# Performance work log

Measured on AMD Instinct MI355X. Metric: run time of the kernel, lower is better.

## Reference

```python
import jax, jax.numpy as jnp
import numpy as np

G = 4          # moe_groups
EPG = 4        # experts per group = e_num // moe_groups
E = 16         # e_num
KG = 2         # moe_max_groups
K = 2          # moe_max_k
GTP = 0.9      # moe_group_top_p
TP = 0.9       # moe_top_p
SCALE = 1.0 / float(np.sqrt(G))  # group_scale


def setup_inputs() -> dict:
    key = jax.random.key(0)
    ks = jax.random.split(key, 6)
    B, T, D, H = 2, 1024, 512, 2048  # H = 4*emb_dim per SwiGLU_FFN(emb_dim, 4*emb_dim)
    x = jax.random.normal(ks[0], (B, T, D), jnp.float32)
    Wr = jax.random.normal(ks[1], (D, G), jnp.float32) * 0.02      # group_router weight
    br = jnp.zeros((G,), jnp.float32)                               # group_router bias
    Wgate = jax.random.normal(ks[2], (G, D, EPG), jnp.float32) * 0.02  # per-group gates
    bgate = jnp.zeros((G, EPG), jnp.float32)
    W1 = jax.random.normal(ks[3], (E, D, H), jnp.float32) * 0.02   # SwiGLU gate proj
    W3 = jax.random.normal(ks[4], (E, D, H), jnp.float32) * 0.02   # SwiGLU up proj
    W2 = jax.random.normal(ks[5], (E, H, D), jnp.float32) * 0.02   # SwiGLU down proj
    return {"x": x, "Wr": Wr, "br": br, "Wgate": Wgate, "bgate": bgate,
            "W1": W1, "W3": W3, "W2": W2}


def _routing_weights(xf, Wr, br, Wgate, bgate):
    # Returns combined per-(token, expert) weight (N, E): group_renorm * expert_renorm * SCALE.
    N = xf.shape[0]
    # ---- group-level top-p routing ----
    gp = jax.nn.softmax(xf @ Wr + br, axis=-1)                      # (N, G)
    order = jnp.argsort(-gp, axis=-1)
    sp_k = jnp.take_along_axis(gp, order, axis=-1)[:, :KG]          # top-KG probs, descending
    idx_k = order[:, :KG]
    act = jnp.cumsum(sp_k, axis=-1) <= GTP
    act = act.at[:, 0].set(True)                                    # always keep best group
    mp = sp_k * act
    rn = mp / (jnp.sum(mp, axis=-1, keepdims=True) + 1e-9)
    w_group = jnp.zeros((N, G), xf.dtype).at[jnp.arange(N)[:, None], idx_k].set(rn)
    # ---- expert-level top-p routing within each group ----
    ep = jax.nn.softmax(jnp.einsum('nd,gde->nge', xf, Wgate) + bgate, axis=-1)  # (N, G, EPG)
    eorder = jnp.argsort(-ep, axis=-1)
    esp = jnp.take_along_axis(ep, eorder, axis=-1)[:, :, :K]
    eidx = eorder[:, :, :K]
    eact = jnp.cumsum(esp, axis=-1) <= TP
    eact = eact.at[:, :, 0].set(True)                               # always keep best expert
    emp = esp * eact
    ern = emp / (jnp.sum(emp, axis=-1, keepdims=True) + 1e-9)
    w_exp = jnp.zeros((N, G, EPG), xf.dtype).at[
        jnp.arange(N)[:, None, None], jnp.arange(G)[None, :, None], eidx].set(ern)
    return (w_group[:, :, None] * w_exp * SCALE).reshape(N, E)      # (N, E)


def reference(x, Wr, br, Wgate, bgate, W1, W3, W2):
    B, T, D = x.shape
    xf = x.reshape(-1, D)                                           # (N, D)
    tw = _routing_weights(xf, Wr, br, Wgate, bgate)                 # (N, E)
    out = jnp.zeros_like(xf)
    for e in range(E):  # fixed structural loop over experts
        h = jax.nn.silu(xf @ W1[e]) * (xf @ W3[e])                  # SwiGLU hidden (N, H)
        out = out + tw[:, e:e + 1] * (h @ W2[e])
    return out.reshape(B, T, D)
```

## Files before the change

kernel.cpp:

```cpp
#include <hip/hip_runtime.h>
#include <math.h>

typedef unsigned short u16;
typedef unsigned int   u32;
typedef short s16x8 __attribute__((ext_vector_type(8)));
typedef float f32x4 __attribute__((ext_vector_type(4)));

#define N_TOK 2048
#define DIM   512
#define HID   2048
#define NE    16
#define NG    4
#define EPG   4
#define MAXT  2048

#define BM 64
#define BN 128
#define BK 64

#define WS_CNT    0
#define WS_OFF    128
#define WS_TOKIDX 256
#define WS_TW     (WS_TOKIDX + NE*MAXT*4)
#define WS_XB     (WS_TW + N_TOK*NE*4)
#define WS_HBUF   (WS_XB + (size_t)N_TOK*DIM*2)
#define WS_W1T    (WS_HBUF + (size_t)8192*HID*2)
#define WS_W3T    (WS_W1T + (size_t)NE*HID*DIM*2)
#define WS_W2T    (WS_W3T + (size_t)NE*HID*DIM*2)

__device__ __forceinline__ int* ws_i32(void* ws, size_t off) { return (int*)((char*)ws + off); }

__device__ __forceinline__ u16 f2b(float f) {
    union { float f; u32 i; } v; v.f = f;
    u32 b = v.i;
    u32 r = b + 0x7FFFu + ((b >> 16) & 1u);
    return (u16)(r >> 16);
}

__device__ __forceinline__ void gl_lds16(const u16* g, u16* l) {
    __builtin_amdgcn_global_load_lds((const __attribute__((address_space(1))) void*)g,
                                     (__attribute__((address_space(3))) void*)l, 16, 0, 0);
}

__global__ __launch_bounds__(256) void routing_kernel(
    const float* __restrict__ x, const float* __restrict__ Wr, const float* __restrict__ br,
    const float* __restrict__ Wgate, const float* __restrict__ bgate, void* ws)
{
    int tid = threadIdx.x;
    int t = blockIdx.x * 4 + (tid >> 6);
    int lane = tid & 63;

    float xl[8];
    {
        const float4* xr = (const float4*)(x + (size_t)t*DIM + lane*8);
        float4 a = xr[0], b = xr[1];
        xl[0]=a.x; xl[1]=a.y; xl[2]=a.z; xl[3]=a.w;
        xl[4]=b.x; xl[5]=b.y; xl[6]=b.z; xl[7]=b.w;
    }

    {
        union { u16 h[8]; uint4 q; } pk;
        #pragma unroll
        for (int i = 0; i < 8; i++) pk.h[i] = f2b(xl[i]);
        u16* xb = (u16*)((char*)ws + WS_XB);
        *(uint4*)(xb + (size_t)t*DIM + lane*8) = pk.q;
    }

    float gl[NG] = {0.f,0.f,0.f,0.f};
    float el[NE];
    #pragma unroll
    for (int e = 0; e < NE; e++) el[e] = 0.f;

    {
        const float4* Wr4 = (const float4*)Wr;
        #pragma unroll
        for (int c = 0; c < 8; c++) {
            float4 w = Wr4[lane*8 + c];
            gl[0] += xl[c]*w.x; gl[1] += xl[c]*w.y;
            gl[2] += xl[c]*w.z; gl[3] += xl[c]*w.w;
        }
    }
    {
        const float4* Wg4 = (const float4*)Wgate;
        #pragma unroll
        for (int g = 0; g < NG; g++) {
            #pragma unroll
            for (int c = 0; c < 8; c++) {
                float4 w = Wg4[(size_t)g*DIM + lane*8 + c];
                el[g*4+0] += xl[c]*w.x; el[g*4+1] += xl[c]*w.y;
                el[g*4+2] += xl[c]*w.z; el[g*4+3] += xl[c]*w.w;
            }
        }
    }

    #pragma unroll
    for (int g = 0; g < NG; g++)
        #pragma unroll
        for (int s = 32; s; s >>= 1) gl[g] += __shfl_xor(gl[g], s);
    #pragma unroll
    for (int e = 0; e < NE; e++)
        #pragma unroll
        for (int s = 32; s; s >>= 1) el[e] += __shfl_xor(el[e], s);

    if (lane != 0) return;

    float gp[NG];
    float mx = -1e30f;
    #pragma unroll
    for (int g = 0; g < NG; g++) { gl[g] += br[g]; mx = fmaxf(mx, gl[g]); }
    float sum = 0.f;
    #pragma unroll
    for (int g = 0; g < NG; g++) { gp[g] = expf(gl[g] - mx); sum += gp[g]; }
    #pragma unroll
    for (int g = 0; g < NG; g++) gp[g] /= sum;

    int i0 = 0;
    #pragma unroll
    for (int g = 1; g < NG; g++) if (gp[g] > gp[i0]) i0 = g;
    int i1 = -1;
    #pragma unroll
    for (int g = 0; g < NG; g++) { if (g == i0) continue; if (i1 < 0 || gp[g] > gp[i1]) i1 = g; }

    bool act1 = (gp[i0] + gp[i1]) <= 0.9f;
    float mp0 = gp[i0], mp1 = act1 ? gp[i1] : 0.f;
    float inv = 1.f / (mp0 + mp1 + 1e-9f);
    float wg[NG] = {0.f,0.f,0.f,0.f};
    wg[i0] = mp0 * inv;
    wg[i1] = mp1 * inv;

    float tw[NE];
    #pragma unroll
    for (int g = 0; g < NG; g++) {
        float ep[EPG];
        float emx = -1e30f;
        #pragma unroll
        for (int j = 0; j < EPG; j++) {
            float v = el[g*4 + j] + bgate[g*4 + j];
            ep[j] = v; emx = fmaxf(emx, v);
        }
        float es = 0.f;
        #pragma unroll
        for (int j = 0; j < EPG; j++) { ep[j] = expf(ep[j] - emx); es += ep[j]; }
        #pragma unroll
        for (int j = 0; j < EPG; j++) ep[j] /= es;

        int j0 = 0;
        #pragma unroll
        for (int j = 1; j < EPG; j++) if (ep[j] > ep[j0]) j0 = j;
        int j1 = -1;
        #pragma unroll
        for (int j = 0; j < EPG; j++) { if (j == j0) continue; if (j1 < 0 || ep[j] > ep[j1]) j1 = j; }

        bool ea1 = (ep[j0] + ep[j1]) <= 0.9f;
        float e0 = ep[j0], e1 = ea1 ? ep[j1] : 0.f;
        float einv = 1.f / (e0 + e1 + 1e-9f);
        float we[EPG] = {0.f,0.f,0.f,0.f};
        we[j0] = e0 * einv;
        we[j1] = e1 * einv;
        #pragma unroll
        for (int j = 0; j < EPG; j++) tw[g*4 + j] = wg[g] * we[j] * 0.5f;
    }

    float* twT = (float*)((char*)ws + WS_TW);
    #pragma unroll
    for (int e = 0; e < NE; e++) twT[(size_t)e*N_TOK + t] = tw[e];
}

__global__ __launch_bounds__(1024) void expert_scan_kernel(void* ws)
{
    int tid = threadIdx.x;
    int e = tid >> 6, lane = tid & 63;
    const float* twT = (const float*)((char*)ws + WS_TW) + (size_t)e*N_TOK;
    int* tok = ws_i32(ws, WS_TOKIDX) + e*MAXT;
    __shared__ int scnt[NE];

    float v[32];
    #pragma unroll
    for (int r = 0; r < 32; r++) v[r] = twT[r*64 + lane];

    unsigned long long lanemask = (1ull << lane) - 1ull;
    int base = 0;
    #pragma unroll
    for (int r = 0; r < 32; r++) {
        bool a = v[r] > 0.f;
        unsigned long long m = __ballot(a);
        if (a) tok[base + __popcll(m & lanemask)] = r*64 + lane;
        base += __popcll(m);
    }
    if (lane == 0) scnt[e] = base;
    __syncthreads();
    if (tid == 0) {
        int* cnt = ws_i32(ws, WS_CNT);
        int* off = ws_i32(ws, WS_OFF);
        int s = 0;
        for (int i = 0; i < NE; i++) { cnt[i] = scnt[i]; off[i] = s; s += scnt[i]; }
        off[NE] = s;
    }
}

__global__ __launch_bounds__(256) void transpose_all_kernel(
    const float* __restrict__ W1, const float* __restrict__ W3,
    const float* __restrict__ W2, void* ws)
{
    int z = blockIdx.z;
    int mat = z >> 4, e = z & 15;
    const float* src; u16* dst; int K, N, k0, n0;
    if (mat == 0)      { src = W1; dst = (u16*)((char*)ws + WS_W1T); K = DIM; N = HID; n0 = blockIdx.x*64; k0 = blockIdx.y*64; }
    else if (mat == 1) { src = W3; dst = (u16*)((char*)ws + WS_W3T); K = DIM; N = HID; n0 = blockIdx.x*64; k0 = blockIdx.y*64; }
    else               { src = W2; dst = (u16*)((char*)ws + WS_W2T); K = HID; N = DIM; k0 = blockIdx.x*64; n0 = blockIdx.y*64; }

    const float* s = src + (size_t)e*K*N;
    u16* d = dst + (size_t)e*N*K;

    __shared__ u16 T[64*64];
    int tid = threadIdx.x;
    int j = tid & 15, i = tid >> 4;

    {
        const float* base = s + (size_t)(k0 + 4*i)*N + n0 + 4*j;
        float4 v0 = *(const float4*)(base);
        float4 v1 = *(const float4*)(base + N);
        float4 v2 = *(const float4*)(base + 2*N);
        float4 v3 = *(const float4*)(base + 3*N);
        int swz = (j & 7) << 1;
        int pc = 4 * (i ^ swz);
        union { u16 h[4]; uint2 q; } p;
        p.h[0]=f2b(v0.x); p.h[1]=f2b(v1.x); p.h[2]=f2b(v2.x); p.h[3]=f2b(v3.x);
        *(uint2*)(&T[(4*j+0)*64 + pc]) = p.q;
        p.h[0]=f2b(v0.y); p.h[1]=f2b(v1.y); p.h[2]=f2b(v2.y); p.h[3]=f2b(v3.y);
        *(uint2*)(&T[(4*j+1)*64 + pc]) = p.q;
        p.h[0]=f2b(v0.z); p.h[1]=f2b(v1.z); p.h[2]=f2b(v2.z); p.h[3]=f2b(v3.z);
        *(uint2*)(&T[(4*j+2)*64 + pc]) = p.q;
        p.h[0]=f2b(v0.w); p.h[1]=f2b(v1.w); p.h[2]=f2b(v2.w); p.h[3]=f2b(v3.w);
        *(uint2*)(&T[(4*j+3)*64 + pc]) = p.q;
    }
    __syncthreads();
    #pragma unroll
    for (int it = 0; it < 2; it++) {
        int idx = tid + it*256;
        int nr = idx >> 3, sg = idx & 7;
        int p = (2*sg) ^ (((nr >> 2) & 7) << 1);
        *(s16x8*)(d + (size_t)(n0+nr)*K + k0 + sg*8) = *(const s16x8*)(&T[nr*64 + 4*p]);
    }
}

__global__ __launch_bounds__(256) void gemm1_fast(void* ws)
{
    int e  = blockIdx.z;
    const int* cnt = ws_i32(ws, WS_CNT);
    int ce = cnt[e];
    int m0 = blockIdx.y * BM;
    if (m0 >= ce) return;
    int n0 = blockIdx.x * BN;

    const int* off = ws_i32(ws, WS_OFF);
    const int* tok = ws_i32(ws, WS_TOKIDX) + e*MAXT;
    const u16* xb  = (const u16*)((char*)ws + WS_XB);
    const u16* W1T = (const u16*)((char*)ws + WS_W1T) + (size_t)e*HID*DIM;
    const u16* W3T = (const u16*)((char*)ws + WS_W3T) + (size_t)e*HID*DIM;
    u16* hbuf = (u16*)((char*)ws + WS_HBUF);
    int obase = off[e] + m0;

    __shared__ u16 As[BM*BK];
    __shared__ u16 Bs0[BN*BK];
    __shared__ u16 Bs1[BN*BK];
    __shared__ int rowtok[BM];

    int tid = threadIdx.x;
    if (tid < BM) {
        int m = m0 + tid;
        rowtok[tid] = tok[m < ce ? m : (ce - 1)];
    }
    __syncthreads();

    int wave = tid >> 6, lane = tid & 63;
    int quad = lane >> 4, l16 = lane & 15;
    int swz  = l16 & 7;
    int r8 = lane >> 3, sg = lane & 7;
    int swk = ((sg ^ r8) << 3);

    const u16* arow0 = xb + (size_t)rowtok[wave*16 + r8]*DIM + swk;
    const u16* arow1 = xb + (size_t)rowtok[wave*16 + 8 + r8]*DIM + swk;
    const u16* b1row[4]; const u16* b3row[4];
    #pragma unroll
    for (int i = 0; i < 4; i++) {
        size_t nr = (size_t)(n0 + wave*32 + i*8 + r8)*DIM + swk;
        b1row[i] = W1T + nr;
        b3row[i] = W3T + nr;
    }

    f32x4 acc1[4][2], acc3[4][2];
    #pragma unroll
    for (int mt = 0; mt < 4; mt++)
        #pragma unroll
        for (int nt = 0; nt < 2; nt++) {
            acc1[mt][nt] = (f32x4){0.f,0.f,0.f,0.f};
            acc3[mt][nt] = (f32x4){0.f,0.f,0.f,0.f};
        }

    for (int k0 = 0; k0 < DIM; k0 += BK) {
        gl_lds16(arow0 + k0, &As[(wave*16)*BK]);
        gl_lds16(arow1 + k0, &As[(wave*16 + 8)*BK]);
        #pragma unroll
        for (int i = 0; i < 4; i++) {
            gl_lds16(b1row[i] + k0, &Bs0[(wave*32 + i*8)*BK]);
            gl_lds16(b3row[i] + k0, &Bs1[(wave*32 + i*8)*BK]);
        }
        __syncthreads();

        #pragma unroll
        for (int kk = 0; kk < BK; kk += 32) {
            int jj = (kk >> 3) + quad;
            int so = ((jj ^ swz) << 3);
            s16x8 af[4];
            #pragma unroll
            for (int mt = 0; mt < 4; mt++)
                af[mt] = *(const s16x8*)(&As[(mt*16 + l16)*BK + so]);
            #pragma unroll
            for (int nt = 0; nt < 2; nt++) {
                int n = wave*32 + nt*16 + l16;
                s16x8 b1 = *(const s16x8*)(&Bs0[n*BK + so]);
                s16x8 b3 = *(const s16x8*)(&Bs1[n*BK + so]);
                #pragma unroll
                for (int mt = 0; mt < 4; mt++) {
                    acc1[mt][nt] = __builtin_amdgcn_mfma_f32_16x16x32_bf16(af[mt], b1, acc1[mt][nt], 0, 0, 0);
                    acc3[mt][nt] = __builtin_amdgcn_mfma_f32_16x16x32_bf16(af[mt], b3, acc3[mt][nt], 0, 0, 0);
                }
            }
        }
        __syncthreads();
    }

    #pragma unroll
    for (int mt = 0; mt < 4; mt++) {
        #pragma unroll
        for (int r = 0; r < 4; r++) {
            int row = mt*16 + quad*4 + r;
            if (m0 + row < ce) {
                #pragma unroll
                for (int nt = 0; nt < 2; nt++) {
                    float a = acc1[mt][nt][r];
                    float b = acc3[mt][nt][r];
                    float h = (a / (1.f + expf(-a))) * b;
                    int col = wave*32 + nt*16 + l16;
                    hbuf[(size_t)(obase + row)*HID + n0 + col] = f2b(h);
                }
            }
        }
    }
}

__global__ __launch_bounds__(256) void gemm2_fast(void* ws, float* __restrict__ out)
{
    int e  = blockIdx.z;
    const int* cnt = ws_i32(ws, WS_CNT);
    int ce = cnt[e];
    int m0 = blockIdx.y * BM;
    if (m0 >= ce) return;
    int n0 = blockIdx.x * BN;

    const int* off = ws_i32(ws, WS_OFF);
    const int* tok = ws_i32(ws, WS_TOKIDX) + e*MAXT;
    const float* twT = (const float*)((char*)ws + WS_TW);
    const u16* hbuf = (const u16*)((char*)ws + WS_HBUF);
    const u16* W2T = (const u16*)((char*)ws + WS_W2T) + (size_t)e*DIM*HID;
    int abase = off[e] + m0;
    int total = off[NE];

    __shared__ u16 As[BM*BK];
    __shared__ u16 Bs[BN*BK];

    int tid = threadIdx.x;
    int wave = tid >> 6, lane = tid & 63;
    int quad = lane >> 4, l16 = lane & 15;
    int swz  = l16 & 7;
    int r8 = lane >> 3, sg = lane & 7;
    int swk = ((sg ^ r8) << 3);

    int ar0 = abase + wave*16 + r8;      if (ar0 > total - 1) ar0 = total - 1;
    int ar1 = abase + wave*16 + 8 + r8;  if (ar1 > total - 1) ar1 = total - 1;
    const u16* arow0 = hbuf + (size_t)ar0*HID + swk;
    const u16* arow1 = hbuf + (size_t)ar1*HID + swk;
    const u16* brow[4];
    #pragma unroll
    for (int i = 0; i < 4; i++)
        brow[i] = W2T + (size_t)(n0 + wave*32 + i*8 + r8)*HID + swk;

    f32x4 acc[4][2];
    #pragma unroll
    for (int mt = 0; mt < 4; mt++)
        #pragma unroll
        for (int nt = 0; nt < 2; nt++) acc[mt][nt] = (f32x4){0.f,0.f,0.f,0.f};

    for (int k0 = 0; k0 < HID; k0 += BK) {
        gl_lds16(arow0 + k0, &As[(wave*16)*BK]);
        gl_lds16(arow1 + k0, &As[(wave*16 + 8)*BK]);
        #pragma unroll
        for (int i = 0; i < 4; i++)
            gl_lds16(brow[i] + k0, &Bs[(wave*32 + i*8)*BK]);
        __syncthreads();

        #pragma unroll
        for (int kk = 0; kk < BK; kk += 32) {
            int jj = (kk >> 3) + quad;
            int so = ((jj ^ swz) << 3);
            s16x8 af[4];
            #pragma unroll
            for (int mt = 0; mt < 4; mt++)
                af[mt] = *(const s16x8*)(&As[(mt*16 + l16)*BK + so]);
            #pragma unroll
            for (int nt = 0; nt < 2; nt++) {
                int n = wave*32 + nt*16 + l16;
                s16x8 bfr = *(const s16x8*)(&Bs[n*BK + so]);
                #pragma unroll
                for (int mt = 0; mt < 4; mt++)
                    acc[mt][nt] = __builtin_amdgcn_mfma_f32_16x16x32_bf16(af[mt], bfr, acc[mt][nt], 0, 0, 0);
            }
        }
        __syncthreads();
    }

    #pragma unroll
    for (int mt = 0; mt < 4; mt++) {
        #pragma unroll
        for (int r = 0; r < 4; r++) {
            int row = mt*16 + quad*4 + r;
            if (m0 + row < ce) {
                int t = tok[m0 + row];
                float s = twT[(size_t)e*N_TOK + t];
                #pragma unroll
                for (int nt = 0; nt < 2; nt++) {
                    int col = wave*32 + nt*16 + l16;
                    atomicAdd(out + (size_t)t*DIM + n0 + col, acc[mt][nt][r] * s);
                }
            }
        }
    }
}

extern "C" void kernel_launch(void* const* d_in, const int* in_sizes, int n_in,
                              void* d_out, int out_size, void* d_ws, size_t ws_size,
                              hipStream_t stream)
{
    const float* x     = (const float*)d_in[0];
    const float* Wr    = (const float*)d_in[1];
    const float* br    = (const float*)d_in[2];
    const float* Wgate = (const float*)d_in[3];
    const float* bgate = (const float*)d_in[4];
    const float* W1    = (const float*)d_in[5];
    const float* W3    = (const float*)d_in[6];
    const float* W2    = (const float*)d_in[7];
    float* out = (float*)d_out;

    hipMemsetAsync(d_out, 0, (size_t)out_size*sizeof(float), stream);

    transpose_all_kernel<<<dim3(32, 8, 48), 256, 0, stream>>>(W1, W3, W2, d_ws);
    routing_kernel<<<N_TOK/4, 256, 0, stream>>>(x, Wr, br, Wgate, bgate, d_ws);
    expert_scan_kernel<<<1, 1024, 0, stream>>>(d_ws);
    gemm1_fast<<<dim3(HID/BN, N_TOK/BM, NE), 256, 0, stream>>>(d_ws);
    gemm2_fast<<<dim3(DIM/BN, N_TOK/BM, NE), 256, 0, stream>>>(d_ws, out);
}
```

Before: 360.6 us.

## Replace atomic scatter with slot buffer plus gather, enlarge transpose tiles

```diff
diff --git a/kernel.cpp b/kernel.cpp
--- a/kernel.cpp
+++ b/kernel.cpp
@@ -27,6 +27,8 @@
 #define WS_W1T    (WS_HBUF + (size_t)8192*HID*2)
 #define WS_W3T    (WS_W1T + (size_t)NE*HID*DIM*2)
 #define WS_W2T    (WS_W3T + (size_t)NE*HID*DIM*2)
+#define WS_SLOT   (WS_W2T + (size_t)NE*DIM*HID*2)
+#define WS_BUF2   WS_W1T
 
 __device__ __forceinline__ int* ws_i32(void* ws, size_t off) { return (int*)((char*)ws + off); }
 
@@ -173,6 +175,7 @@
     const float* twT = (const float*)((char*)ws + WS_TW) + (size_t)e*N_TOK;
     int* tok = ws_i32(ws, WS_TOKIDX) + e*MAXT;
     __shared__ int scnt[NE];
+    __shared__ int soff[NE+1];
 
     float v[32];
     #pragma unroll
@@ -193,54 +196,69 @@
         int* cnt = ws_i32(ws, WS_CNT);
         int* off = ws_i32(ws, WS_OFF);
         int s = 0;
-        for (int i = 0; i < NE; i++) { cnt[i] = scnt[i]; off[i] = s; s += scnt[i]; }
-        off[NE] = s;
-    }
-}
-
-__global__ __launch_bounds__(256) void transpose_all_kernel(
+        for (int i = 0; i < NE; i++) { cnt[i] = scnt[i]; off[i] = s; soff[i] = s; s += scnt[i]; }
+        off[NE] = s; soff[NE] = s;
+    }
+    __syncthreads();
+
+    int* slot_of = ws_i32(ws, WS_SLOT) + e*N_TOK;
+    int base2 = soff[e];
+    #pragma unroll
+    for (int r = 0; r < 32; r++) {
+        bool a = v[r] > 0.f;
+        unsigned long long m = __ballot(a);
+        int pre = __popcll(m & lanemask);
+        slot_of[r*64 + lane] = a ? (base2 + pre) : -1;
+        base2 += __popcll(m);
+    }
+}
+
+__global__ __launch_bounds__(1024) void transpose_all_kernel(
     const float* __restrict__ W1, const float* __restrict__ W3,
     const float* __restrict__ W2, void* ws)
 {
     int z = blockIdx.z;
     int mat = z >> 4, e = z & 15;
+    int tx = blockIdx.x;
     const float* src; u16* dst; int K, N, k0, n0;
-    if (mat == 0)      { src = W1; dst = (u16*)((char*)ws + WS_W1T); K = DIM; N = HID; n0 = blockIdx.x*64; k0 = blockIdx.y*64; }
-    else if (mat == 1) { src = W3; dst = (u16*)((char*)ws + WS_W3T); K = DIM; N = HID; n0 = blockIdx.x*64; k0 = blockIdx.y*64; }
-    else               { src = W2; dst = (u16*)((char*)ws + WS_W2T); K = HID; N = DIM; k0 = blockIdx.x*64; n0 = blockIdx.y*64; }
+    if (mat == 0)      { src = W1; dst = (u16*)((char*)ws + WS_W1T); K = DIM; N = HID; k0 = (tx>>4)*256; n0 = (tx&15)*128; }
+    else if (mat == 1) { src = W3; dst = (u16*)((char*)ws + WS_W3T); K = DIM; N = HID; k0 = (tx>>4)*256; n0 = (tx&15)*128; }
+    else               { src = W2; dst = (u16*)((char*)ws + WS_W2T); K = HID; N = DIM; k0 = (tx>>2)*256; n0 = (tx&3)*128; }
 
     const float* s = src + (size_t)e*K*N;
     u16* d = dst + (size_t)e*N*K;
 
-    __shared__ u16 T[64*64];
+    __shared__ u16 T[128*256];
     int tid = threadIdx.x;
-    int j = tid & 15, i = tid >> 4;
-
-    {
-        const float* base = s + (size_t)(k0 + 4*i)*N + n0 + 4*j;
+    int j = tid & 31, i0 = tid >> 5;
+
+    #pragma unroll
+    for (int itk = 0; itk < 2; itk++) {
+        int kb = 4*i0 + 128*itk;
+        const float* base = s + (size_t)(k0 + kb)*N + n0 + 4*j;
         float4 v0 = *(const float4*)(base);
         float4 v1 = *(const float4*)(base + N);
         float4 v2 = *(const float4*)(base + 2*N);
         float4 v3 = *(const float4*)(base + 3*N);
-        int swz = (j & 7) << 1;
-        int pc = 4 * (i ^ swz);
+        int c  = (kb >> 2);
+        int pc = 4 * (c ^ ((j & 15) << 1));
         union { u16 h[4]; uint2 q; } p;
         p.h[0]=f2b(v0.x); p.h[1]=f2b(v1.x); p.h[2]=f2b(v2.x); p.h[3]=f2b(v3.x);
-        *(uint2*)(&T[(4*j+0)*64 + pc]) = p.q;
+        *(uint2*)(&T[(4*j+0)*256 + pc]) = p.q;
         p.h[0]=f2b(v0.y); p.h[1]=f2b(v1.y); p.h[2]=f2b(v2.y); p.h[3]=f2b(v3.y);
-        *(uint2*)(&T[(4*j+1)*64 + pc]) = p.q;
+        *(uint2*)(&T[(4*j+1)*256 + pc]) = p.q;
         p.h[0]=f2b(v0.z); p.h[1]=f2b(v1.z); p.h[2]=f2b(v2.z); p.h[3]=f2b(v3.z);
-        *(uint2*)(&T[(4*j+2)*64 + pc]) = p.q;
+        *(uint2*)(&T[(4*j+2)*256 + pc]) = p.q;
         p.h[0]=f2b(v0.w); p.h[1]=f2b(v1.w); p.h[2]=f2b(v2.w); p.h[3]=f2b(v3.w);
-        *(uint2*)(&T[(4*j+3)*64 + pc]) = p.q;
+        *(uint2*)(&T[(4*j+3)*256 + pc]) = p.q;
     }
     __syncthreads();
     #pragma unroll
-    for (int it = 0; it < 2; it++) {
-        int idx = tid + it*256;
-        int nr = idx >> 3, sg = idx & 7;
-        int p = (2*sg) ^ (((nr >> 2) & 7) << 1);
-        *(s16x8*)(d + (size_t)(n0+nr)*K + k0 + sg*8) = *(const s16x8*)(&T[nr*64 + 4*p]);
+    for (int it = 0; it < 4; it++) {
+        int idx = tid + it*1024;
+        int nr = idx >> 5, sg = idx & 31;
+        int cp = (2*sg) ^ (((nr >> 2) & 15) << 1);
+        *(s16x8*)(d + (size_t)(n0+nr)*K + k0 + sg*8) = *(const s16x8*)(&T[nr*256 + 4*cp]);
     }
 }
 
@@ -350,7 +368,7 @@
     }
 }
 
-__global__ __launch_bounds__(256) void gemm2_fast(void* ws, float* __restrict__ out)
+__global__ __launch_bounds__(256) void gemm2_fast(void* ws)
 {
     int e  = blockIdx.z;
     const int* cnt = ws_i32(ws, WS_CNT);
@@ -364,6 +382,7 @@
     const float* twT = (const float*)((char*)ws + WS_TW);
     const u16* hbuf = (const u16*)((char*)ws + WS_HBUF);
     const u16* W2T = (const u16*)((char*)ws + WS_W2T) + (size_t)e*DIM*HID;
+    float* buf2 = (float*)((char*)ws + WS_BUF2);
     int abase = off[e] + m0;
     int total = off[NE];
 
@@ -431,11 +450,31 @@
                 #pragma unroll
                 for (int nt = 0; nt < 2; nt++) {
                     int col = wave*32 + nt*16 + l16;
-                    atomicAdd(out + (size_t)t*DIM + n0 + col, acc[mt][nt][r] * s);
+                    buf2[(size_t)(abase + row)*DIM + n0 + col] = acc[mt][nt][r] * s;
                 }
             }
         }
     }
+}
+
+__global__ __launch_bounds__(128) void gather_kernel(void* ws, float* __restrict__ out)
+{
+    int t = blockIdx.x;
+    int tid = threadIdx.x;
+    const int* slot_of = ws_i32(ws, WS_SLOT);
+    const float* buf2 = (const float*)((char*)ws + WS_BUF2);
+
+    int d = tid * 4;
+    float4 acc = {0.f, 0.f, 0.f, 0.f};
+    #pragma unroll
+    for (int e = 0; e < NE; e++) {
+        int s = slot_of[e*N_TOK + t];
+        if (s >= 0) {
+            float4 v = *(const float4*)(buf2 + (size_t)s*DIM + d);
+            acc.x += v.x; acc.y += v.y; acc.z += v.z; acc.w += v.w;
+        }
+    }
+    *(float4*)(out + (size_t)t*DIM + d) = acc;
 }
 
 extern "C" void kernel_launch(void* const* d_in, const int* in_sizes, int n_in,
@@ -452,11 +491,10 @@
     const float* W2    = (const float*)d_in[7];
     float* out = (float*)d_out;
 
-    hipMemsetAsync(d_out, 0, (size_t)out_size*sizeof(float), stream);
-
-    transpose_all_kernel<<<dim3(32, 8, 48), 256, 0, stream>>>(W1, W3, W2, d_ws);
+    transpose_all_kernel<<<dim3(32, 1, 48), 1024, 0, stream>>>(W1, W3, W2, d_ws);
     routing_kernel<<<N_TOK/4, 256, 0, stream>>>(x, Wr, br, Wgate, bgate, d_ws);
     expert_scan_kernel<<<1, 1024, 0, stream>>>(d_ws);
     gemm1_fast<<<dim3(HID/BN, N_TOK/BM, NE), 256, 0, stream>>>(d_ws);
-    gemm2_fast<<<dim3(DIM/BN, N_TOK/BM, NE), 256, 0, stream>>>(d_ws, out);
-}
+    gemm2_fast<<<dim3(DIM/BN, N_TOK/BM, NE), 256, 0, stream>>>(d_ws);
+    gather_kernel<<<N_TOK, 128, 0, stream>>>(d_ws, out);
+}
```

Result: no change. 359.0 us (-0.5%).
